# Optimization experiments

Measured on AMD Instinct MI355X. Metric: run time of the kernel, lower is better.

Reference implementation:

```python
import jax, jax.numpy as jnp
import numpy as np

N = 50000      # nodes
E = 800000     # edges (avg degree 16)
HN = 32        # hidden_nfeats (out_node_feats per head)
HE = 32        # hidden_efeats (out_edge_feats per head)
H = 3          # num_heads (forced to 3 by hidden*3 input dims)
ODF = 16       # countyodfeats raw edge feature dim
L = 3          # countycount: total number of EGAT layers
NIDX = 4096    # rows selected by idxs


def setup_inputs() -> dict:
    key = jax.random.key(0)
    ks = jax.random.split(key, 18)

    def w(k, shape, fan_in):
        return jax.random.normal(k, shape, jnp.float32) / np.float32(np.sqrt(fan_in))

    return {
        "ndata_h": jax.random.normal(ks[0], (N, H * HN), jnp.float32),
        "countyodfeats": jax.random.normal(ks[1], (E, ODF), jnp.float32),
        "src": jax.random.randint(ks[2], (E,), 0, N, dtype=jnp.int32),
        "dst": jax.random.randint(ks[3], (E,), 0, N, dtype=jnp.int32),
        "idxs": jax.random.randint(ks[4], (NIDX,), 0, N, dtype=jnp.int32),
        # first EGATConv: in_node = H*HN = 96, in_edge = ODF = 16
        "Wns0": w(ks[5], (H * HN, H * HN), H * HN),
        "Wni0": w(ks[6], (H * HN, H * HE), H * HN),
        "Wfij0": w(ks[7], (ODF, H * HE), ODF),
        "Wnj0": w(ks[8], (H * HN, H * HE), H * HN),
        "attn0": w(ks[9], (1, H, HE), HE),
        "bias0": jnp.zeros((H * HE,), jnp.float32),
        # remaining L-1 layers stacked: in_node = H*HN, in_edge = H*HE
        "Wns": w(ks[10], (L - 1, H * HN, H * HN), H * HN),
        "Wni": w(ks[11], (L - 1, H * HN, H * HE), H * HN),
        "Wfij": w(ks[12], (L - 1, H * HE, H * HE), H * HE),
        "Wnj": w(ks[13], (L - 1, H * HN, H * HE), H * HN),
        "attn": w(ks[14], (L - 1, 1, H, HE), HE),
        "bias": jnp.zeros((L - 1, H * HE), jnp.float32),
    }


def _egat_layer(nf, ef, src, dst, Wns, Wni, Wfij, Wnj, attn, bias):
    """Faithful DGL EGATConv forward. nf: [N,Fn], ef: [E,Fe]."""
    # edge feature update: leaky_relu(fc_ni(h_i) + fc_nj(h_j) + fc_fij(e_ij) + b)
    f = (nf @ Wni)[src] + (nf @ Wnj)[dst] + ef @ Wfij + bias  # [E, H*HE]
    f = jax.nn.leaky_relu(f, 0.01).reshape(-1, H, HE)          # [E, H, HE]
    # per-edge attention logits
    e = jnp.einsum("ehd,ohd->eh", f, attn)                      # [E, H]
    # segment softmax over incoming edges of each dst node
    m = jax.ops.segment_max(e, dst, num_segments=N)             # [N, H]
    ex = jnp.exp(e - m[dst])
    s = jax.ops.segment_sum(ex, dst, num_segments=N)
    a = ex / s[dst]                                             # [E, H]
    # gather src node transforms, weight by attention, scatter-add to dst
    h = (nf @ Wns).reshape(-1, H, HN)                           # [N, H, HN]
    msg = h[src] * a[:, :, None]                                # [E, H, HN]
    h_out = jax.ops.segment_sum(msg, dst, num_segments=N)       # [N, H, HN]
    return h_out, f


def reference(ndata_h, countyodfeats, src, dst, idxs,
              Wns0, Wni0, Wfij0, Wnj0, attn0, bias0,
              Wns, Wni, Wfij, Wnj, attn, bias):
    nh, eh = _egat_layer(ndata_h, countyodfeats, src, dst,
                         Wns0, Wni0, Wfij0, Wnj0, attn0, bias0)
    nh = jax.nn.relu(nh.reshape(N, -1))
    eh = jax.nn.relu(eh.reshape(E, -1))
    for i in range(L - 1):
        nh, eh = _egat_layer(nh, eh, src, dst,
                             Wns[i], Wni[i], Wfij[i], Wnj[i], attn[i], bias[i])
        if i != L - 2:
            nh = jax.nn.relu(nh.reshape(N, -1))
            eh = jax.nn.relu(eh.reshape(E, -1))
        else:
            nh = nh.reshape(N, -1)
            eh = eh.reshape(E, -1)
    return nh[idxs, :]
```

## Files before the change

### kernel.cpp

```cpp
#include <hip/hip_runtime.h>
#include <hip/hip_bf16.h>
#include <cstdint>
#include <cstddef>

#define N_NODES 50000
#define N_EDGES 800000
#define NSEL    4096
#define F       96
#define K_ODF   16

typedef __attribute__((ext_vector_type(8))) short  short8;
typedef __attribute__((ext_vector_type(4))) float  floatx4;

using bf16 = __hip_bfloat16;

__device__ inline float b2f(bf16 x){ return __bfloat162float(x); }
__device__ inline bf16  f2b(float x){ return __float2bfloat16(x); }
__device__ inline short f2bs(float x){ return __builtin_bit_cast(short, __float2bfloat16(x)); }
__device__ inline int clampi(int v, int hi){ return v < 0 ? 0 : (v >= hi ? hi-1 : v); }

__device__ inline unsigned int addpk_bf16(unsigned int a, unsigned int b){
  float alo = __builtin_bit_cast(float, a<<16);
  float ahi = __builtin_bit_cast(float, a & 0xffff0000u);
  float blo = __builtin_bit_cast(float, b<<16);
  float bhi = __builtin_bit_cast(float, b & 0xffff0000u);
  unsigned int pl = (unsigned int)(unsigned short)f2bs(alo+blo);
  unsigned int ph = (unsigned int)(unsigned short)f2bs(ahi+bhi);
  return pl | (ph<<16);
}

struct F32S {
  using T = float;
  static constexpr size_t bytes = 4;
  static __device__ short8 ld8(const T* p){
    float4 u = *(const float4*)p;
    float4 v = *(const float4*)(p+4);
    short8 r;
    r[0]=f2bs(u.x); r[1]=f2bs(u.y); r[2]=f2bs(u.z); r[3]=f2bs(u.w);
    r[4]=f2bs(v.x); r[5]=f2bs(v.y); r[6]=f2bs(v.z); r[7]=f2bs(v.w);
    return r;
  }
  static __device__ short8 lds_ld(const char*){ return short8{0,0,0,0,0,0,0,0}; }
  static __device__ void lds_st(char*, float){}
};
struct BF16S {
  using T = bf16;
  static constexpr size_t bytes = 2;
  static __device__ short8 ld8(const T* p){ return *(const short8*)p; }
  static __device__ short8 lds_ld(const char* p){ return *(const short8*)p; }
  static __device__ void lds_st(char* p, float v){ *(bf16*)p = f2b(v); }
};
struct FP8S {
  using T = unsigned char;
  static constexpr size_t bytes = 1;
  static __device__ short8 cvt8(int2 w){
    short8 r;
    r[0]=f2bs(__builtin_amdgcn_cvt_f32_fp8(w.x,0));
    r[1]=f2bs(__builtin_amdgcn_cvt_f32_fp8(w.x,1));
    r[2]=f2bs(__builtin_amdgcn_cvt_f32_fp8(w.x,2));
    r[3]=f2bs(__builtin_amdgcn_cvt_f32_fp8(w.x,3));
    r[4]=f2bs(__builtin_amdgcn_cvt_f32_fp8(w.y,0));
    r[5]=f2bs(__builtin_amdgcn_cvt_f32_fp8(w.y,1));
    r[6]=f2bs(__builtin_amdgcn_cvt_f32_fp8(w.y,2));
    r[7]=f2bs(__builtin_amdgcn_cvt_f32_fp8(w.y,3));
    return r;
  }
  static __device__ short8 ld8(const T* p){ return cvt8(*(const int2*)p); }
  static __device__ short8 lds_ld(const char* p){ return cvt8(*(const int2*)p); }
  static __device__ void lds_st(char* p, float v){
    int pk = __builtin_amdgcn_cvt_pk_fp8_f32(v, 0.f, 0, false);
    *(unsigned char*)p = (unsigned char)(pk & 0xff);
  }
};

struct WP { const float* p[12]; };
#define WT_ELEMS (11*9216 + 1536)

__global__ void k_prep(WP w, bf16* __restrict__ Wt){
  int g = blockIdx.x*blockDim.x + threadIdx.x;
  if (g >= WT_ELEMS) return;
  float v;
  if (g < 11*9216){
    int id = g / 9216, s = g % 9216;
    int c = s / 96, k = s % 96;
    v = w.p[id][k*96 + c];
  } else {
    int s = g - 11*9216;
    int c = s / 16, k = s % 16;
    v = w.p[11][k*96 + c];
  }
  Wt[g] = f2b(v);
}

__global__ void k_count(const int* __restrict__ dst, int* __restrict__ counts){
  int e = blockIdx.x*blockDim.x + threadIdx.x;
  if (e < N_EDGES) atomicAdd(&counts[clampi(dst[e], N_NODES)], 1);
}

__global__ void k_scan(const int* __restrict__ counts, int* __restrict__ row_ptr){
  const int T = 1024;
  const int n = N_NODES;
  int tid = threadIdx.x;
  int seg = (n + T - 1)/T;
  int start = tid*seg;
  int end = (start+seg < n) ? start+seg : n;
  int s = 0;
  for (int i=start;i<end;i++) s += counts[i];
  __shared__ int wsums[16];
  int lane = tid & 63, wid = tid >> 6;
  int v = s;
  #pragma unroll
  for (int off=1; off<64; off<<=1){
    int t = __shfl_up(v, off);
    if (lane >= off) v += t;
  }
  if (lane==63) wsums[wid] = v;
  __syncthreads();
  if (wid==0 && lane < 16){
    int w = wsums[lane];
    #pragma unroll
    for (int off=1; off<16; off<<=1){
      int t = __shfl_up(w, off);
      if (lane>=off) w += t;
    }
    wsums[lane] = w;
  }
  __syncthreads();
  int base = (wid>0 ? wsums[wid-1] : 0) + (v - s);
  int run = base;
  for (int i=start;i<end;i++){ row_ptr[i] = run; run += counts[i]; }
  if (tid==T-1) row_ptr[n] = run;
}

__global__ void k_fill(const int* __restrict__ dst, const int* __restrict__ row_ptr,
                       int* __restrict__ cursor, int* __restrict__ csr_e){
  int e = blockIdx.x*blockDim.x + threadIdx.x;
  if (e < N_EDGES){
    int t = clampi(dst[e], N_NODES);
    int pos = atomicAdd(&cursor[t], 1);
    int idx = row_ptr[t] + pos;
    if (idx >= 0 && idx < N_EDGES) csr_e[idx] = e;
  }
}

template<class AS>
__global__ __launch_bounds__(256) void k_node_gemm(
    const typename AS::T* A,
    const bf16* __restrict__ Wt_ni, const bf16* __restrict__ Wt_nj, const bf16* __restrict__ Wt_ns,
    bf16* __restrict__ NI, bf16* __restrict__ NJ, bf16* __restrict__ HS)
{
  const bf16* Wt; bf16* O;
  if (blockIdx.z==0){ Wt=Wt_ni; O=NI; } else if (blockIdx.z==1){ Wt=Wt_nj; O=NJ; } else { Wt=Wt_ns; O=HS; }
  int wave = threadIdx.x >> 6, lane = threadIdx.x & 63;
  int lo = lane & 15, q = lane >> 4;
  int m0 = (blockIdx.x*4 + wave)*16;
  int n0 = blockIdx.y*16;
  int row = m0 + lo; if (row >= N_NODES) row = N_NODES-1;
  floatx4 acc = {0.f,0.f,0.f,0.f};
  #pragma unroll
  for (int kb=0; kb<3; kb++){
    int k0 = kb*32 + q*8;
    short8 a = AS::ld8(A + (size_t)row*F + k0);
    short8 b = *(const short8*)(Wt + (size_t)(n0+lo)*96 + k0);
    acc = __builtin_amdgcn_mfma_f32_16x16x32_bf16(a,b,acc,0,0,0);
  }
  #pragma unroll
  for (int r=0;r<4;r++){
    int m = m0 + q*4 + r;
    if (m < N_NODES) O[(size_t)m*F + n0+lo] = f2b(acc[r]);
  }
}

template<int K_IN, bool STORE_EF, class INS, class OUTS>
__global__ __launch_bounds__(256) void k_edge4(
    const typename INS::T* EF, const bf16* __restrict__ Wt,
    const bf16* __restrict__ NI, const bf16* __restrict__ NJ,
    const float* __restrict__ bias, const float* __restrict__ attn,
    const int* __restrict__ src, const int* __restrict__ dst,
    typename OUTS::T* EFO, float* __restrict__ logits)
{
  __shared__ __align__(16) char lds_ef[4][3328];
  __shared__ __align__(16) char lds_g[4][3328];
  __shared__ __align__(16) float lstage[4][48];

  int wave = threadIdx.x >> 6, lane = threadIdx.x & 63;
  int lo = lane & 15, q = lane >> 4;
  size_t e0 = ((size_t)blockIdx.x*4 + wave)*16;
  char* myl = lds_ef[wave];
  char* gl  = lds_g[wave];

  #pragma unroll
  for (int j=0;j<3;j++){
    int chunk = j*64 + lane;
    int er = chunk/12, c16 = chunk%12;
    int se = clampi(src[e0+er], N_NODES);
    int de = clampi(dst[e0+er], N_NODES);
    uint4 a = *(const uint4*)((const char*)NI + (size_t)se*192 + c16*16);
    uint4 b = *(const uint4*)((const char*)NJ + (size_t)de*192 + c16*16);
    uint4 g;
    g.x = addpk_bf16(a.x,b.x); g.y = addpk_bf16(a.y,b.y);
    g.z = addpk_bf16(a.z,b.z); g.w = addpk_bf16(a.w,b.w);
    *(uint4*)(gl + er*208 + c16*16) = g;
  }

  short8 afr[(K_IN+31)/32];
  if constexpr (K_IN == 96){
    constexpr int RS  = 96*(int)INS::bytes + 16;
    constexpr int CPR = (96*(int)INS::bytes)/16;
    #pragma unroll
    for (int j=0; j*64 < 16*CPR; j++){
      int chunk = j*64 + lane;
      if ((16*CPR) % 64 == 0 || chunk < 16*CPR){
        int er = chunk / CPR, c16 = chunk % CPR;
        int4 v = *(const int4*)((const char*)EF + ((size_t)(e0+er)*96)*INS::bytes + (size_t)c16*16);
        *(int4*)(myl + er*RS + c16*16) = v;
      }
    }
    #pragma unroll
    for (int kb=0; kb<3; kb++)
      afr[kb] = INS::lds_ld(myl + lo*RS + (kb*32 + q*8)*(int)INS::bytes);
  } else {
    if (q < 2) afr[0] = INS::ld8(EF + (size_t)(e0+lo)*K_IN + q*8);
    else       afr[0] = short8{0,0,0,0,0,0,0,0};
  }

  float hsum[3][4] = {{0.f,0.f,0.f,0.f},{0.f,0.f,0.f,0.f},{0.f,0.f,0.f,0.f}};
  constexpr int ORS = 96*(int)OUTS::bytes + 16;

  #pragma unroll
  for (int t=0; t<6; t++){
    int col = t*16 + lo;
    floatx4 acc = {0.f,0.f,0.f,0.f};
    if constexpr (K_IN == 96){
      #pragma unroll
      for (int kb=0; kb<3; kb++){
        short8 b = *(const short8*)(Wt + (size_t)col*96 + kb*32 + q*8);
        acc = __builtin_amdgcn_mfma_f32_16x16x32_bf16(afr[kb], b, acc, 0,0,0);
      }
    } else {
      short8 b = (q<2) ? *(const short8*)(Wt + (size_t)col*16 + q*8)
                       : short8{0,0,0,0,0,0,0,0};
      acc = __builtin_amdgcn_mfma_f32_16x16x32_bf16(afr[0], b, acc, 0,0,0);
    }
    float aw = attn[col];
    float bv = bias[col];
    #pragma unroll
    for (int r=0;r<4;r++){
      float gv = b2f(*(const bf16*)(gl + (q*4+r)*208 + col*2));
      float pre = acc[r] + gv + bv;
      if constexpr (STORE_EF)
        OUTS::lds_st(myl + (q*4+r)*ORS + col*(int)OUTS::bytes, fmaxf(pre, 0.f));
      float lk = pre > 0.f ? pre : 0.01f*pre;
      hsum[t>>1][r] += lk*aw;
    }
  }

  #pragma unroll
  for (int h=0;h<3;h++){
    #pragma unroll
    for (int r=0;r<4;r++){
      float v = hsum[h][r];
      v += __shfl_xor(v,1);
      v += __shfl_xor(v,2);
      v += __shfl_xor(v,4);
      v += __shfl_xor(v,8);
      if (lo==0) lstage[wave][(q*4+r)*3 + h] = v;
    }
  }
  if (lane < 12){
    float4 v = *(const float4*)(&lstage[wave][lane*4]);
    *(float4*)((char*)logits + e0*12 + (size_t)lane*16) = v;
  }

  if constexpr (STORE_EF){
    constexpr int OCPR = (96*(int)OUTS::bytes)/16;
    #pragma unroll
    for (int j=0; j*64 < 16*OCPR; j++){
      int chunk = j*64 + lane;
      if ((16*OCPR) % 64 == 0 || chunk < 16*OCPR){
        int er = chunk / OCPR, c16 = chunk % OCPR;
        int4 v = *(const int4*)(myl + er*ORS + c16*16);
        *(int4*)((char*)EFO + ((size_t)(e0+er)*96)*OUTS::bytes + (size_t)c16*16) = v;
      }
    }
  }
}

template<bool RELU>
__global__ __launch_bounds__(256) void k_agg2(
    const float* __restrict__ logits,
    const bf16* __restrict__ HS,
    const int* __restrict__ src,
    const int* __restrict__ row_ptr, const int* __restrict__ csr_e,
    bf16* __restrict__ nf_out)
{
  int wave = threadIdx.x >> 6, lane = threadIdx.x & 63;
  int node = blockIdx.x*4 + wave;
  if (node >= N_NODES) return;
  int r0 = row_ptr[node], r1 = row_ptr[node+1];
  int deg = r1 - r0;

  float m0=-3.0e38f, m1=-3.0e38f, m2=-3.0e38f;
  for (int i = r0 + lane; i < r1; i += 64){
    int e = csr_e[i];
    m0 = fmaxf(m0, logits[(size_t)e*3+0]);
    m1 = fmaxf(m1, logits[(size_t)e*3+1]);
    m2 = fmaxf(m2, logits[(size_t)e*3+2]);
  }
  #pragma unroll
  for (int o=1;o<64;o<<=1){
    m0 = fmaxf(m0, __shfl_xor(m0,o));
    m1 = fmaxf(m1, __shfl_xor(m1,o));
    m2 = fmaxf(m2, __shfl_xor(m2,o));
  }
  float s0=0.f, s1=0.f, s2=0.f;
  for (int i = r0 + lane; i < r1; i += 64){
    int e = csr_e[i];
    s0 += __expf(logits[(size_t)e*3+0] - m0);
    s1 += __expf(logits[(size_t)e*3+1] - m1);
    s2 += __expf(logits[(size_t)e*3+2] - m2);
  }
  #pragma unroll
  for (int o=1;o<64;o<<=1){
    s0 += __shfl_xor(s0,o);
    s1 += __shfl_xor(s1,o);
    s2 += __shfl_xor(s2,o);
  }

  if (lane < 48){
    int h = (2*lane) >> 5;
    float mm = (h==0) ? m0 : (h==1 ? m1 : m2);
    float ss = (h==0) ? s0 : (h==1 ? s1 : s2);
    float invs = (deg > 0) ? 1.0f/ss : 0.f;
    float ax = 0.f, ay = 0.f;
    #pragma unroll 4
    for (int i = r0; i < r1; i++){
      int e = csr_e[i];
      float al = __expf(logits[(size_t)e*3 + h] - mm);
      unsigned int w = *(const unsigned int*)((const char*)HS + (size_t)src[e]*192 + lane*4);
      float x = __builtin_bit_cast(float, w << 16);
      float y = __builtin_bit_cast(float, w & 0xffff0000u);
      ax += al*x; ay += al*y;
    }
    float ox = ax*invs, oy = ay*invs;
    if (RELU){ ox = fmaxf(ox,0.f); oy = fmaxf(oy,0.f); }
    unsigned int lo16 = (unsigned int)(unsigned short)f2bs(ox);
    unsigned int hi16 = (unsigned int)(unsigned short)f2bs(oy);
    *(unsigned int*)((char*)nf_out + (size_t)node*192 + lane*4) = lo16 | (hi16<<16);
  }
}

__global__ void k_gather(const bf16* __restrict__ nf, const int* __restrict__ idxs,
                         float* __restrict__ out){
  int t = blockIdx.x*blockDim.x + threadIdx.x;
  if (t < NSEL*F){
    int i = t / F, c = t % F;
    out[t] = b2f(nf[(size_t)clampi(idxs[i], N_NODES)*F + c]);
  }
}

template<class EFS>
static void run_all(const float* ndata, const float* odfeat, const int* src, const int* dst,
                    const int* idxs,
                    const float* Wns0, const float* Wni0, const float* Wfij0, const float* Wnj0,
                    const float* attn0, const float* bias0,
                    const float* WnsL, const float* WniL, const float* WfijL, const float* WnjL,
                    const float* attnL, const float* biasL,
                    float* out, char* ws, hipStream_t stream)
{
  size_t off = 0;
  auto alloc = [&](size_t bytes)->char*{
    char* p = ws + off; off += (bytes + 255) & ~(size_t)255; return p;
  };
  typename EFS::T* ef = (typename EFS::T*)alloc((size_t)N_EDGES*F*EFS::bytes);
  bf16* NI      = (bf16*)alloc((size_t)N_NODES*F*2);
  bf16* NJ      = (bf16*)alloc((size_t)N_NODES*F*2);
  bf16* HS      = (bf16*)alloc((size_t)N_NODES*F*2);
  bf16* nf      = (bf16*)alloc((size_t)N_NODES*F*2);
  float* logits = (float*)alloc((size_t)N_EDGES*3*4);
  int*  row_ptr = (int*)alloc((size_t)(N_NODES+1)*4);
  int*  counts  = (int*)alloc((size_t)N_NODES*4);
  int*  cursor  = (int*)alloc((size_t)N_NODES*4);
  int*  csr_e   = (int*)alloc((size_t)N_EDGES*4);
  bf16* Wt      = (bf16*)alloc((size_t)WT_ELEMS*2);

  WP wp;
  wp.p[0]=Wni0; wp.p[1]=Wnj0; wp.p[2]=Wns0;
  wp.p[3]=WniL; wp.p[4]=WnjL; wp.p[5]=WnsL; wp.p[6]=WfijL;
  wp.p[7]=WniL+9216; wp.p[8]=WnjL+9216; wp.p[9]=WnsL+9216; wp.p[10]=WfijL+9216;
  wp.p[11]=Wfij0;
  k_prep<<<(WT_ELEMS+255)/256, 256, 0, stream>>>(wp, Wt);

  hipMemsetAsync(counts, 0, (size_t)N_NODES*4, stream);
  hipMemsetAsync(cursor, 0, (size_t)N_NODES*4, stream);
  k_count<<<(N_EDGES+255)/256, 256, 0, stream>>>(dst, counts);
  k_scan<<<1, 1024, 0, stream>>>(counts, row_ptr);
  k_fill<<<(N_EDGES+255)/256, 256, 0, stream>>>(dst, row_ptr, cursor, csr_e);

  dim3 ngrid((N_NODES + 63)/64, F/16, 3);
  int  egrid = N_EDGES/64;
  int  agrid = (N_NODES + 3)/4;

  const bf16 *WtNI0 = Wt,          *WtNJ0 = Wt+9216,   *WtNS0 = Wt+18432;
  const bf16 *WtNI1 = Wt+3*9216,   *WtNJ1 = Wt+4*9216, *WtNS1 = Wt+5*9216, *WtE1 = Wt+6*9216;
  const bf16 *WtNI2 = Wt+7*9216,   *WtNJ2 = Wt+8*9216, *WtNS2 = Wt+9*9216, *WtE2 = Wt+10*9216;
  const bf16 *WtE0  = Wt+11*9216;

  k_node_gemm<F32S><<<ngrid, 256, 0, stream>>>(ndata, WtNI0, WtNJ0, WtNS0, NI, NJ, HS);
  k_edge4<K_ODF, true, F32S, EFS><<<egrid, 256, 0, stream>>>(
      odfeat, WtE0, NI, NJ, bias0, attn0, src, dst, ef, logits);
  k_agg2<true><<<agrid, 256, 0, stream>>>(logits, HS, src, row_ptr, csr_e, nf);

  k_node_gemm<BF16S><<<ngrid, 256, 0, stream>>>(nf, WtNI1, WtNJ1, WtNS1, NI, NJ, HS);
  k_edge4<F, true, EFS, EFS><<<egrid, 256, 0, stream>>>(
      ef, WtE1, NI, NJ, biasL, attnL, src, dst, ef, logits);
  k_agg2<true><<<agrid, 256, 0, stream>>>(logits, HS, src, row_ptr, csr_e, nf);

  k_node_gemm<BF16S><<<ngrid, 256, 0, stream>>>(nf, WtNI2, WtNJ2, WtNS2, NI, NJ, HS);
  k_edge4<F, false, EFS, EFS><<<egrid, 256, 0, stream>>>(
      ef, WtE2, NI, NJ, biasL+F, attnL+F, src, dst, (typename EFS::T*)nullptr, logits);
  k_agg2<false><<<agrid, 256, 0, stream>>>(logits, HS, src, row_ptr, csr_e, nf);

  k_gather<<<(NSEL*F + 255)/256, 256, 0, stream>>>(nf, idxs, out);
}

extern "C" void kernel_launch(void* const* d_in, const int* in_sizes, int n_in,
                              void* d_out, int out_size, void* d_ws, size_t ws_size,
                              hipStream_t stream)
{
  (void)in_sizes; (void)n_in; (void)out_size;
  const float* ndata  = (const float*)d_in[0];
  const float* odfeat = (const float*)d_in[1];
  const int*   src    = (const int*)d_in[2];
  const int*   dst    = (const int*)d_in[3];
  const int*   idxs   = (const int*)d_in[4];
  const float* Wns0   = (const float*)d_in[5];
  const float* Wni0   = (const float*)d_in[6];
  const float* Wfij0  = (const float*)d_in[7];
  const float* Wnj0   = (const float*)d_in[8];
  const float* attn0  = (const float*)d_in[9];
  const float* bias0  = (const float*)d_in[10];
  const float* WnsL   = (const float*)d_in[11];
  const float* WniL   = (const float*)d_in[12];
  const float* WfijL  = (const float*)d_in[13];
  const float* WnjL   = (const float*)d_in[14];
  const float* attnL  = (const float*)d_in[15];
  const float* biasL  = (const float*)d_in[16];

  bool planA = ws_size >= (size_t)206000000;
  if (planA)
    run_all<BF16S>(ndata, odfeat, src, dst, idxs, Wns0, Wni0, Wfij0, Wnj0, attn0, bias0,
                   WnsL, WniL, WfijL, WnjL, attnL, biasL,
                   (float*)d_out, (char*)d_ws, stream);
  else
    run_all<FP8S>(ndata, odfeat, src, dst, idxs, Wns0, Wni0, Wfij0, Wnj0, attn0, bias0,
                  WnsL, WniL, WfijL, WnjL, attnL, biasL,
                  (float*)d_out, (char*)d_ws, stream);
}
```

Measured before the change: 946.0 us.

## Process edges in dst-sorted order and compute softmax max with atomics in edge kernel

The edge kernel now walks edges in CSR (dst-sorted) order through the permutation and stores logits and edge features in that order. The per-destination softmax max is produced in the edge kernel with float-keyed atomicMax into spare bytes of the nf buffer. The aggregation kernel then drops its separate max and sum passes, reading logits contiguously and accumulating the sum inline. This removes two gather passes per node, at the cost of indirect reads in the edge kernel, atomics, an extra init kernel per layer, and aliasing of the max buffer into nf's unused tail bytes.

```diff
diff --git a/kernel.cpp b/kernel.cpp
--- a/kernel.cpp
+++ b/kernel.cpp
@@ -18,6 +18,15 @@
 __device__ inline bf16  f2b(float x){ return __float2bfloat16(x); }
 __device__ inline short f2bs(float x){ return __builtin_bit_cast(short, __float2bfloat16(x)); }
 __device__ inline int clampi(int v, int hi){ return v < 0 ? 0 : (v >= hi ? hi-1 : v); }
+
+__device__ inline unsigned fkey(float f){
+  unsigned b = __builtin_bit_cast(unsigned, f);
+  return (b & 0x80000000u) ? ~b : (b | 0x80000000u);
+}
+__device__ inline float funkey(unsigned k){
+  unsigned b = (k & 0x80000000u) ? (k & 0x7fffffffu) : ~k;
+  return __builtin_bit_cast(float, b);
+}
 
 __device__ inline unsigned int addpk_bf16(unsigned int a, unsigned int b){
   float alo = __builtin_bit_cast(float, a<<16);
@@ -143,6 +152,14 @@
   }
 }
 
+__global__ void k_maxinit(unsigned* nfm){
+  int t = blockIdx.x*blockDim.x + threadIdx.x;
+  if (t < N_NODES*3){
+    int n = t/3, h = t - n*3;
+    *(unsigned*)((char*)nfm + (size_t)n*192 + 180 + h*4) = 0u;
+  }
+}
+
 template<class AS>
 __global__ __launch_bounds__(256) void k_node_gemm(
     const typename AS::T* A,
@@ -172,12 +189,13 @@
 }
 
 template<int K_IN, bool STORE_EF, class INS, class OUTS>
-__global__ __launch_bounds__(256) void k_edge4(
+__global__ __launch_bounds__(256) void k_edge5(
     const typename INS::T* EF, const bf16* __restrict__ Wt,
     const bf16* __restrict__ NI, const bf16* __restrict__ NJ,
     const float* __restrict__ bias, const float* __restrict__ attn,
     const int* __restrict__ src, const int* __restrict__ dst,
-    typename OUTS::T* EFO, float* __restrict__ logits)
+    const int* __restrict__ perm,
+    typename OUTS::T* EFO, float* __restrict__ logits, unsigned* nfmax)
 {
   __shared__ __align__(16) char lds_ef[4][3328];
   __shared__ __align__(16) char lds_g[4][3328];
@@ -185,18 +203,21 @@
 
   int wave = threadIdx.x >> 6, lane = threadIdx.x & 63;
   int lo = lane & 15, q = lane >> 4;
-  size_t e0 = ((size_t)blockIdx.x*4 + wave)*16;
+  size_t p0 = ((size_t)blockIdx.x*4 + wave)*16;
   char* myl = lds_ef[wave];
   char* gl  = lds_g[wave];
 
+  int eL[3], seL[3], deL[3];
+  #pragma unroll
+  for (int j=0;j<3;j++) eL[j] = perm[p0 + (j*64+lane)/12];
+  #pragma unroll
+  for (int j=0;j<3;j++){ seL[j] = clampi(src[eL[j]], N_NODES); deL[j] = clampi(dst[eL[j]], N_NODES); }
   #pragma unroll
   for (int j=0;j<3;j++){
     int chunk = j*64 + lane;
-    int er = chunk/12, c16 = chunk%12;
-    int se = clampi(src[e0+er], N_NODES);
-    int de = clampi(dst[e0+er], N_NODES);
-    uint4 a = *(const uint4*)((const char*)NI + (size_t)se*192 + c16*16);
-    uint4 b = *(const uint4*)((const char*)NJ + (size_t)de*192 + c16*16);
+    int er = chunk/12, c16 = chunk - er*12;
+    uint4 a = *(const uint4*)((const char*)NI + (size_t)seL[j]*192 + c16*16);
+    uint4 b = *(const uint4*)((const char*)NJ + (size_t)deL[j]*192 + c16*16);
     uint4 g;
     g.x = addpk_bf16(a.x,b.x); g.y = addpk_bf16(a.y,b.y);
     g.z = addpk_bf16(a.z,b.z); g.w = addpk_bf16(a.w,b.w);
@@ -212,7 +233,7 @@
       int chunk = j*64 + lane;
       if ((16*CPR) % 64 == 0 || chunk < 16*CPR){
         int er = chunk / CPR, c16 = chunk % CPR;
-        int4 v = *(const int4*)((const char*)EF + ((size_t)(e0+er)*96)*INS::bytes + (size_t)c16*16);
+        int4 v = *(const int4*)((const char*)EF + ((p0+er)*96)*INS::bytes + (size_t)c16*16);
         *(int4*)(myl + er*RS + c16*16) = v;
       }
     }
@@ -220,7 +241,8 @@
     for (int kb=0; kb<3; kb++)
       afr[kb] = INS::lds_ld(myl + lo*RS + (kb*32 + q*8)*(int)INS::bytes);
   } else {
-    if (q < 2) afr[0] = INS::ld8(EF + (size_t)(e0+lo)*K_IN + q*8);
+    int pe = perm[p0 + lo];
+    if (q < 2) afr[0] = INS::ld8(EF + (size_t)pe*K_IN + q*8);
     else       afr[0] = short8{0,0,0,0,0,0,0,0};
   }
 
@@ -255,6 +277,7 @@
     }
   }
 
+  float red[3][4];
   #pragma unroll
   for (int h=0;h<3;h++){
     #pragma unroll
@@ -264,12 +287,27 @@
       v += __shfl_xor(v,2);
       v += __shfl_xor(v,4);
       v += __shfl_xor(v,8);
-      if (lo==0) lstage[wave][(q*4+r)*3 + h] = v;
+      red[h][r] = v;
+    }
+  }
+  {
+    float sel = red[0][0];
+    #pragma unroll
+    for (int h=0;h<3;h++)
+      #pragma unroll
+      for (int r=0;r<4;r++)
+        if (h*4+r != 0) sel = (lo == h*4+r) ? red[h][r] : sel;
+    if (lo < 12){
+      int hh = lo >> 2, rr = lo & 3;
+      lstage[wave][(q*4+rr)*3 + hh] = sel;
+      int e = perm[p0 + q*4 + rr];
+      int n = clampi(dst[e], N_NODES);
+      atomicMax((unsigned*)((char*)nfmax + (size_t)n*192 + 180 + hh*4), fkey(sel));
     }
   }
   if (lane < 12){
     float4 v = *(const float4*)(&lstage[wave][lane*4]);
-    *(float4*)((char*)logits + e0*12 + (size_t)lane*16) = v;
+    *(float4*)((char*)logits + p0*12 + (size_t)lane*16) = v;
   }
 
   if constexpr (STORE_EF){
@@ -280,74 +318,46 @@
       if ((16*OCPR) % 64 == 0 || chunk < 16*OCPR){
         int er = chunk / OCPR, c16 = chunk % OCPR;
         int4 v = *(const int4*)(myl + er*ORS + c16*16);
-        *(int4*)((char*)EFO + ((size_t)(e0+er)*96)*OUTS::bytes + (size_t)c16*16) = v;
+        *(int4*)((char*)EFO + ((p0+er)*96)*OUTS::bytes + (size_t)c16*16) = v;
       }
     }
   }
 }
 
 template<bool RELU>
-__global__ __launch_bounds__(256) void k_agg2(
+__global__ __launch_bounds__(256) void k_agg3(
     const float* __restrict__ logits,
     const bf16* __restrict__ HS,
     const int* __restrict__ src,
-    const int* __restrict__ row_ptr, const int* __restrict__ csr_e,
-    bf16* __restrict__ nf_out)
+    const int* __restrict__ row_ptr, const int* __restrict__ perm,
+    const unsigned* nfmax, bf16* nf_out)
 {
   int wave = threadIdx.x >> 6, lane = threadIdx.x & 63;
   int node = blockIdx.x*4 + wave;
-  if (node >= N_NODES) return;
+  if (node >= N_NODES || lane >= 48) return;
   int r0 = row_ptr[node], r1 = row_ptr[node+1];
-  int deg = r1 - r0;
-
-  float m0=-3.0e38f, m1=-3.0e38f, m2=-3.0e38f;
-  for (int i = r0 + lane; i < r1; i += 64){
-    int e = csr_e[i];
-    m0 = fmaxf(m0, logits[(size_t)e*3+0]);
-    m1 = fmaxf(m1, logits[(size_t)e*3+1]);
-    m2 = fmaxf(m2, logits[(size_t)e*3+2]);
-  }
-  #pragma unroll
-  for (int o=1;o<64;o<<=1){
-    m0 = fmaxf(m0, __shfl_xor(m0,o));
-    m1 = fmaxf(m1, __shfl_xor(m1,o));
-    m2 = fmaxf(m2, __shfl_xor(m2,o));
-  }
-  float s0=0.f, s1=0.f, s2=0.f;
-  for (int i = r0 + lane; i < r1; i += 64){
-    int e = csr_e[i];
-    s0 += __expf(logits[(size_t)e*3+0] - m0);
-    s1 += __expf(logits[(size_t)e*3+1] - m1);
-    s2 += __expf(logits[(size_t)e*3+2] - m2);
-  }
-  #pragma unroll
-  for (int o=1;o<64;o<<=1){
-    s0 += __shfl_xor(s0,o);
-    s1 += __shfl_xor(s1,o);
-    s2 += __shfl_xor(s2,o);
-  }
-
-  if (lane < 48){
+  float ox = 0.f, oy = 0.f;
+  if (r1 > r0){
     int h = (2*lane) >> 5;
-    float mm = (h==0) ? m0 : (h==1 ? m1 : m2);
-    float ss = (h==0) ? s0 : (h==1 ? s1 : s2);
-    float invs = (deg > 0) ? 1.0f/ss : 0.f;
-    float ax = 0.f, ay = 0.f;
+    unsigned k = *(const unsigned*)((const char*)nfmax + (size_t)node*192 + 180 + h*4);
+    float m = funkey(k);
+    float ax = 0.f, ay = 0.f, ss = 0.f;
     #pragma unroll 4
     for (int i = r0; i < r1; i++){
-      int e = csr_e[i];
-      float al = __expf(logits[(size_t)e*3 + h] - mm);
-      unsigned int w = *(const unsigned int*)((const char*)HS + (size_t)src[e]*192 + lane*4);
+      float al = __expf(logits[(size_t)i*3 + h] - m);
+      int e = perm[i];
+      unsigned w = *(const unsigned*)((const char*)HS + (size_t)clampi(src[e],N_NODES)*192 + lane*4);
       float x = __builtin_bit_cast(float, w << 16);
       float y = __builtin_bit_cast(float, w & 0xffff0000u);
-      ax += al*x; ay += al*y;
-    }
-    float ox = ax*invs, oy = ay*invs;
+      ax += al*x; ay += al*y; ss += al;
+    }
+    float invs = 1.0f/ss;
+    ox = ax*invs; oy = ay*invs;
     if (RELU){ ox = fmaxf(ox,0.f); oy = fmaxf(oy,0.f); }
-    unsigned int lo16 = (unsigned int)(unsigned short)f2bs(ox);
-    unsigned int hi16 = (unsigned int)(unsigned short)f2bs(oy);
-    *(unsigned int*)((char*)nf_out + (size_t)node*192 + lane*4) = lo16 | (hi16<<16);
-  }
+  }
+  unsigned lo16 = (unsigned)(unsigned short)f2bs(ox);
+  unsigned hi16 = (unsigned)(unsigned short)f2bs(oy);
+  *(unsigned*)((char*)nf_out + (size_t)node*192 + lane*4) = lo16 | (hi16<<16);
 }
 
 __global__ void k_gather(const bf16* __restrict__ nf, const int* __restrict__ idxs,
@@ -383,6 +393,7 @@
   int*  cursor  = (int*)alloc((size_t)N_NODES*4);
   int*  csr_e   = (int*)alloc((size_t)N_EDGES*4);
   bf16* Wt      = (bf16*)alloc((size_t)WT_ELEMS*2);
+  unsigned* nfmax = (unsigned*)nf;
 
   WP wp;
   wp.p[0]=Wni0; wp.p[1]=Wnj0; wp.p[2]=Wns0;
@@ -400,6 +411,7 @@
   dim3 ngrid((N_NODES + 63)/64, F/16, 3);
   int  egrid = N_EDGES/64;
   int  agrid = (N_NODES + 3)/4;
+  int  mgrid = (N_NODES*3 + 255)/256;
 
   const bf16 *WtNI0 = Wt,          *WtNJ0 = Wt+9216,   *WtNS0 = Wt+18432;
   const bf16 *WtNI1 = Wt+3*9216,   *WtNJ1 = Wt+4*9216, *WtNS1 = Wt+5*9216, *WtE1 = Wt+6*9216;
@@ -407,19 +419,22 @@
   const bf16 *WtE0  = Wt+11*9216;
 
   k_node_gemm<F32S><<<ngrid, 256, 0, stream>>>(ndata, WtNI0, WtNJ0, WtNS0, NI, NJ, HS);
-  k_edge4<K_ODF, true, F32S, EFS><<<egrid, 256, 0, stream>>>(
-      odfeat, WtE0, NI, NJ, bias0, attn0, src, dst, ef, logits);
-  k_agg2<true><<<agrid, 256, 0, stream>>>(logits, HS, src, row_ptr, csr_e, nf);
+  k_maxinit<<<mgrid, 256, 0, stream>>>(nfmax);
+  k_edge5<K_ODF, true, F32S, EFS><<<egrid, 256, 0, stream>>>(
+      odfeat, WtE0, NI, NJ, bias0, attn0, src, dst, csr_e, ef, logits, nfmax);
+  k_agg3<true><<<agrid, 256, 0, stream>>>(logits, HS, src, row_ptr, csr_e, nfmax, nf);
 
   k_node_gemm<BF16S><<<ngrid, 256, 0, stream>>>(nf, WtNI1, WtNJ1, WtNS1, NI, NJ, HS);
-  k_edge4<F, true, EFS, EFS><<<egrid, 256, 0, stream>>>(
-      ef, WtE1, NI, NJ, biasL, attnL, src, dst, ef, logits);
-  k_agg2<true><<<agrid, 256, 0, stream>>>(logits, HS, src, row_ptr, csr_e, nf);
+  k_maxinit<<<mgrid, 256, 0, stream>>>(nfmax);
+  k_edge5<F, true, EFS, EFS><<<egrid, 256, 0, stream>>>(
+      ef, WtE1, NI, NJ, biasL, attnL, src, dst, csr_e, ef, logits, nfmax);
+  k_agg3<true><<<agrid, 256, 0, stream>>>(logits, HS, src, row_ptr, csr_e, nfmax, nf);
 
   k_node_gemm<BF16S><<<ngrid, 256, 0, stream>>>(nf, WtNI2, WtNJ2, WtNS2, NI, NJ, HS);
-  k_edge4<F, false, EFS, EFS><<<egrid, 256, 0, stream>>>(
-      ef, WtE2, NI, NJ, biasL+F, attnL+F, src, dst, (typename EFS::T*)nullptr, logits);
-  k_agg2<false><<<agrid, 256, 0, stream>>>(logits, HS, src, row_ptr, csr_e, nf);
+  k_maxinit<<<mgrid, 256, 0, stream>>>(nfmax);
+  k_edge5<F, false, EFS, EFS><<<egrid, 256, 0, stream>>>(
+      ef, WtE2, NI, NJ, biasL+F, attnL+F, src, dst, csr_e, (typename EFS::T*)nullptr, logits, nfmax);
+  k_agg3<false><<<agrid, 256, 0, stream>>>(logits, HS, src, row_ptr, csr_e, nfmax, nf);
 
   k_gather<<<(NSEL*F + 255)/256, 256, 0, stream>>>(nf, idxs, out);
 }
```

After: 1.110 ms. 1.17x slower.
